# Kernel tuning notes

Hardware: AMD Instinct MI355X
Metric: run time of the kernel (lower is better)

The kernel has to match this reference:

```python
import jax, jax.numpy as jnp
import numpy as np

B, X, Y, C, H = 16, 64, 64, 256, 8
N = X * Y
EPS_LN, EPS_BN = 1e-6, 1e-5

def _conv3x3(x, w):
    return jax.lax.conv_general_dilated(x, w, (1, 1), 'SAME', dimension_numbers=('NCHW', 'OIHW', 'NCHW'))

def _bn(x, g, b, m, v):
    # eval-mode BatchNorm2d with running stats
    s = g / jnp.sqrt(v + EPS_BN)
    return x * s[None, :, None, None] + (b - m * s)[None, :, None, None]

def _ln(x, g, b):
    mu = jnp.mean(x, -1, keepdims=True)
    var = jnp.mean((x - mu) ** 2, -1, keepdims=True)
    return (x - mu) * jax.lax.rsqrt(var + EPS_LN) * g + b

def _rotate_half(x):
    x1, x2 = jnp.split(x, 2, axis=-1)
    return jnp.concatenate([-x2, x1], axis=-1)

def _rope(t, f):
    return t * jnp.cos(f) + _rotate_half(t) * jnp.sin(f)

def setup_inputs() -> dict:
    key = jax.random.key(0)
    ks = jax.random.split(key, 9)
    p = {}
    p['input'] = jax.random.normal(ks[0], (B, X, Y), jnp.float32)
    p['freq_x'] = jax.random.normal(ks[1], (B, N, C // 2), jnp.float32)
    p['freq_y'] = jax.random.normal(ks[2], (B, N, C // 2), jnp.float32)
    p['conv1_w'] = jax.random.normal(ks[3], (C, 1, 3, 3), jnp.float32) * 0.1
    p['conv2_w'] = jax.random.normal(ks[4], (C, C, 3, 3), jnp.float32) * 0.02
    for nm in ('bn1', 'bn2'):
        p[nm + '_g'] = jnp.ones((C,), jnp.float32)
        p[nm + '_b'] = jnp.zeros((C,), jnp.float32)
        p[nm + '_m'] = jnp.zeros((C,), jnp.float32)
        p[nm + '_v'] = jnp.ones((C,), jnp.float32)
    p['ln1_g'] = jnp.ones((C,), jnp.float32); p['ln1_b'] = jnp.zeros((C,), jnp.float32)
    p['ln2_g'] = jnp.ones((C,), jnp.float32); p['ln2_b'] = jnp.zeros((C,), jnp.float32)
    p['qkv_w'] = jax.random.normal(ks[5], (3 * C, C), jnp.float32) * 0.02
    p['out_w'] = jax.random.normal(ks[6], (C, C), jnp.float32) * 0.02
    p['out_b'] = jnp.zeros((C,), jnp.float32)
    p['mlp_w1'] = jax.random.normal(ks[7], (C, C), jnp.float32) * 0.02
    p['mlp_b1'] = jnp.zeros((C,), jnp.float32)
    p['mlp_w2'] = jax.random.normal(ks[8], (C, C), jnp.float32) * 0.02
    p['mlp_b2'] = jnp.zeros((C,), jnp.float32)
    return p

def reference(input, freq_x, freq_y, conv1_w, conv2_w, bn1_g, bn1_b, bn1_m, bn1_v, bn2_g, bn2_b, bn2_m, bn2_v, ln1_g, ln1_b, ln2_g, ln2_b, qkv_w, out_w, out_b, mlp_w1, mlp_b1, mlp_w2, mlp_b2):
    x4 = input[:, None]  # [B,1,X,Y]
    out = jax.nn.relu(_bn(_conv3x3(x4, conv1_w), bn1_g, bn1_b, bn1_m, bn1_v))
    out = jax.nn.relu(_bn(_conv3x3(out, conv2_w), bn2_g, bn2_b, bn2_m, bn2_v))
    feat = jax.nn.relu(x4 + out)  # broadcast residual add, [B,C,X,Y]
    inp = feat.transpose(0, 2, 3, 1).reshape(B, N, C)  # 'b h x y -> b (x y) h'
    # --- attention/MLP branch (computed as in source; its result is discarded) ---
    x = _ln(inp, ln1_g, ln1_b)
    tx, ty = x[..., :C // 2], x[..., C // 2:]
    x = jnp.concatenate([_rope(tx, freq_x), _rope(ty, freq_y)], -1)
    qkv = x @ qkv_w.T  # [B,N,3C]
    q, k, v = jnp.split(qkv, 3, -1)
    def _heads(t):
        return t.reshape(B, N, H, C // H).transpose(0, 2, 1, 3)  # [B,H,N,Dh]
    q, k, v = _heads(q), _heads(k), _heads(v)
    q = jax.nn.softmax(q, -1) * ((C // H) ** -0.5)
    k = jax.nn.softmax(k, -2)
    ctx = jnp.einsum('bhnd,bhne->bhde', k, v)   # [B,H,Dh,Dh]
    o = jnp.einsum('bhnd,bhde->bhne', q, ctx)   # [B,H,N,Dh]
    o = o.transpose(0, 2, 1, 3).reshape(B, N, C) @ out_w.T + out_b
    x = o + inp
    y = _ln(x, ln2_g, ln2_b)
    y = jax.nn.gelu(y @ mlp_w1.T + mlp_b1, approximate=False) @ mlp_w2.T + mlp_b2
    x = x + y
    # source module returns `input` (the post-stem tokens), not `x`
    return inp
```

## Files before the change

### kernel.cpp

```cpp
#include <hip/hip_runtime.h>
#include <hip/hip_bf16.h>

#define BB 16
#define XY 64
#define CC 256
#define PD 66

typedef __attribute__((ext_vector_type(8))) short short8;
typedef __attribute__((ext_vector_type(4))) float f32x4;
typedef __hip_bfloat16 bf16;

__device__ __forceinline__ void glds16(const void* g, void* l) {
  __builtin_amdgcn_global_load_lds(
      (const __attribute__((address_space(1))) void*)g,
      (__attribute__((address_space(3))) void*)l, 16, 0, 0);
}

__global__ __launch_bounds__(256) void k_conv1(
    const float* __restrict__ in,
    const float* __restrict__ w1,
    const float* __restrict__ g, const float* __restrict__ bbias,
    const float* __restrict__ m, const float* __restrict__ v,
    bf16* __restrict__ act)
{
  int blk = blockIdx.x;
  int b = blk / PD, hp = blk % PD;
  int c = threadIdx.x;
  bf16* actrow = act + (size_t)(b * PD + hp) * PD * CC;
  if (hp == 0 || hp == PD - 1) {
    for (int wp = 0; wp < PD; ++wp) actrow[wp * CC + c] = __float2bfloat16(0.f);
    return;
  }
  __shared__ float inrow[3][PD];
  int h = hp - 1;
  for (int t = threadIdx.x; t < 3 * PD; t += 256) {
    int r = t / PD, x = t % PD;
    int hr = h - 1 + r, wr = x - 1;
    inrow[r][x] = (hr >= 0 && hr < XY && wr >= 0 && wr < XY)
                      ? in[(b * XY + hr) * XY + wr] : 0.f;
  }
  __syncthreads();
  float w[9];
#pragma unroll
  for (int t = 0; t < 9; ++t) w[t] = w1[c * 9 + t];
  float s  = g[c] * rsqrtf(v[c] + 1e-5f);
  float tt = bbias[c] - m[c] * s;
  actrow[c] = __float2bfloat16(0.f);
  actrow[(PD - 1) * CC + c] = __float2bfloat16(0.f);
  for (int wp = 1; wp <= XY; ++wp) {
    float o = 0.f;
#pragma unroll
    for (int dy = 0; dy < 3; ++dy)
#pragma unroll
      for (int dx = 0; dx < 3; ++dx)
        o = fmaf(inrow[dy][wp - 1 + dx], w[dy * 3 + dx], o);
    actrow[wp * CC + c] = __float2bfloat16(fmaxf(fmaf(o, s, tt), 0.f));
  }
}

__global__ __launch_bounds__(256) void k_wb(
    const float* __restrict__ w2,
    const float* __restrict__ g, const float* __restrict__ v,
    bf16* __restrict__ Wb)
{
  int e = blockIdx.x * 256 + threadIdx.x;
  int j   = e & 7;
  int co  = (e >> 3) & 255;
  int qq  = (e >> 11) & 3;
  int c   = (e >> 13) & 7;
  int tap = e >> 16;
  int ci = c * 32 + qq * 8 + j;
  float s = g[co] * rsqrtf(v[co] + 1e-5f);
  Wb[e] = __float2bfloat16(w2[((size_t)co * CC + ci) * 9 + tap] * s);
}

__global__ __launch_bounds__(256, 3) void k_conv2(
    const bf16* __restrict__ act,
    const bf16* __restrict__ Wb,
    const float* __restrict__ in,
    const float* __restrict__ g2, const float* __restrict__ b2,
    const float* __restrict__ m2, const float* __restrict__ v2,
    float* __restrict__ out)
{
  __shared__ alignas(16) bf16 As[3 * 4 * PD * 8];
  __shared__ alignas(16) bf16 Ws[4 * CC * 8];
  __shared__ float inrow[XY];

  int blk = blockIdx.x;
  int b = blk >> 6, h = blk & 63;
  int tid = threadIdx.x;
  int lane = tid & 63, wv = tid >> 6;
  int m = lane & 15, q = lane >> 4;

  f32x4 acc[4][4];
#pragma unroll
  for (int i = 0; i < 4; ++i)
#pragma unroll
    for (int j = 0; j < 4; ++j) acc[i][j] = f32x4{0.f, 0.f, 0.f, 0.f};

  if (tid < XY) inrow[tid] = in[(b * XY + h) * XY + tid];

  const bf16* actbase = act + (size_t)(b * PD + h) * PD * CC;

  for (int c = 0; c < 8; ++c) {
    for (int tap = 0; tap < 9; ++tap) {
      const bf16* wsrc = Wb + (size_t)(tap * 8 + c) * 8192;
#pragma unroll
      for (int i = 0; i < 4; ++i) {
        int seg = wv * 4 + i;
        glds16((const char*)wsrc + seg * 1024 + lane * 16,
               (char*)Ws + seg * 1024);
      }
      if (tap == 0) {
        for (int idx = tid; idx < 792; idx += 256) {
          int qq = idx & 3, p = idx >> 2;
          int r = p / PD, wp = p % PD;
          short8 val = *(const short8*)(actbase + (size_t)(r * PD + wp) * CC + c * 32 + qq * 8);
          *(short8*)&As[((r * 4 + qq) * PD + wp) * 8] = val;
        }
      }
      __syncthreads();

      int dy = tap / 3, dx = tap % 3;
      short8 af[4], bfr[4];
#pragma unroll
      for (int mt = 0; mt < 4; ++mt)
        af[mt] = *(const short8*)&As[((dy * 4 + q) * PD + mt * 16 + m + dx) * 8];
#pragma unroll
      for (int nt = 0; nt < 4; ++nt)
        bfr[nt] = *(const short8*)&Ws[(q * CC + wv * 64 + nt * 16 + m) * 8];
#pragma unroll
      for (int mt = 0; mt < 4; ++mt)
#pragma unroll
        for (int nt = 0; nt < 4; ++nt)
          acc[mt][nt] = __builtin_amdgcn_mfma_f32_16x16x32_bf16(
              af[mt], bfr[nt], acc[mt][nt], 0, 0, 0);
      __syncthreads();
    }
  }

  float t2[4];
#pragma unroll
  for (int nt = 0; nt < 4; ++nt) {
    int co = wv * 64 + nt * 16 + m;
    float s2 = g2[co] * rsqrtf(v2[co] + 1e-5f);
    t2[nt] = b2[co] - m2[co] * s2;
  }
  float* ob = out + (size_t)(b * XY + h) * XY * CC;
#pragma unroll
  for (int mt = 0; mt < 4; ++mt)
#pragma unroll
    for (int r = 0; r < 4; ++r) {
      int wp = mt * 16 + q * 4 + r;
      float iv = inrow[wp];
#pragma unroll
      for (int nt = 0; nt < 4; ++nt) {
        int co = wv * 64 + nt * 16 + m;
        float val = fmaxf(acc[mt][nt][r] + t2[nt], 0.f);
        ob[(size_t)wp * CC + co] = fmaxf(iv + val, 0.f);
      }
    }
}

extern "C" void kernel_launch(void* const* d_in, const int* in_sizes, int n_in,
                              void* d_out, int out_size, void* d_ws, size_t ws_size,
                              hipStream_t stream) {
  const float* in_   = (const float*)d_in[0];
  const float* w1    = (const float*)d_in[3];
  const float* w2    = (const float*)d_in[4];
  const float* bn1_g = (const float*)d_in[5];
  const float* bn1_b = (const float*)d_in[6];
  const float* bn1_m = (const float*)d_in[7];
  const float* bn1_v = (const float*)d_in[8];
  const float* bn2_g = (const float*)d_in[9];
  const float* bn2_b = (const float*)d_in[10];
  const float* bn2_m = (const float*)d_in[11];
  const float* bn2_v = (const float*)d_in[12];
  float* out = (float*)d_out;

  bf16* act = (bf16*)d_ws;
  bf16* Wb  = act + (size_t)BB * PD * PD * CC;

  k_conv1<<<BB * PD, 256, 0, stream>>>(in_, w1, bn1_g, bn1_b, bn1_m, bn1_v, act);
  k_wb<<<(9 * CC * CC) / 256, 256, 0, stream>>>(w2, bn2_g, bn2_v, Wb);
  k_conv2<<<BB * XY, 256, 0, stream>>>(act, Wb, in_, bn2_g, bn2_b, bn2_m, bn2_v, out);
}
```

Measured before the change: 102.8 us.

## Restructure conv2 into 4-row tiles with triple-buffered weights and channel-group layout

The activation layout changes to channel-group-major [b][row][32 groups][66][8] so conv2 can stage A tiles directly with global_load_lds. conv1 now computes 8 channels per thread. conv2 now uses 512-thread blocks, each covering 4 output rows, with an 8x4 accumulator per wave. Weights for K=64 chunks are triple-buffered and prefetched two taps ahead, and MFMAs are interleaved with LDS loads under manual waitcnt and barriers plus setprio. Blocks are also swizzled across XCDs. The aim is to raise reuse of weights and activations and to overlap global loads with MFMA work, at the cost of higher register pressure and fragile hand-written synchronization.

```diff
diff --git a/kernel.cpp b/kernel.cpp
--- a/kernel.cpp
+++ b/kernel.cpp
@@ -4,7 +4,7 @@
 #define BB 16
 #define XY 64
 #define CC 256
-#define PD 66
+#define PR 66
 
 typedef __attribute__((ext_vector_type(8))) short short8;
 typedef __attribute__((ext_vector_type(4))) float f32x4;
@@ -24,37 +24,57 @@
     bf16* __restrict__ act)
 {
   int blk = blockIdx.x;
-  int b = blk / PD, hp = blk % PD;
-  int c = threadIdx.x;
-  bf16* actrow = act + (size_t)(b * PD + hp) * PD * CC;
-  if (hp == 0 || hp == PD - 1) {
-    for (int wp = 0; wp < PD; ++wp) actrow[wp * CC + c] = __float2bfloat16(0.f);
+  int b = blk / PR, prow = blk % PR;
+  short8* base = (short8*)(act + (size_t)(b * PR + prow) * 32 * PR * 8);
+  int tid = threadIdx.x;
+  short8 z8 = {0, 0, 0, 0, 0, 0, 0, 0};
+  if (prow == 0 || prow == PR - 1) {
+    for (int i = tid; i < 32 * PR; i += 256) base[i] = z8;
     return;
   }
-  __shared__ float inrow[3][PD];
-  int h = hp - 1;
-  for (int t = threadIdx.x; t < 3 * PD; t += 256) {
-    int r = t / PD, x = t % PD;
+  __shared__ float inrow[3][PR];
+  int h = prow - 1;
+  for (int t = tid; t < 3 * PR; t += 256) {
+    int r = t / PR, x = t % PR;
     int hr = h - 1 + r, wr = x - 1;
     inrow[r][x] = (hr >= 0 && hr < XY && wr >= 0 && wr < XY)
                       ? in[(b * XY + hr) * XY + wr] : 0.f;
   }
   __syncthreads();
-  float w[9];
-#pragma unroll
-  for (int t = 0; t < 9; ++t) w[t] = w1[c * 9 + t];
-  float s  = g[c] * rsqrtf(v[c] + 1e-5f);
-  float tt = bbias[c] - m[c] * s;
-  actrow[c] = __float2bfloat16(0.f);
-  actrow[(PD - 1) * CC + c] = __float2bfloat16(0.f);
-  for (int wp = 1; wp <= XY; ++wp) {
-    float o = 0.f;
-#pragma unroll
-    for (int dy = 0; dy < 3; ++dy)
-#pragma unroll
-      for (int dx = 0; dx < 3; ++dx)
-        o = fmaf(inrow[dy][wp - 1 + dx], w[dy * 3 + dx], o);
-    actrow[wp * CC + c] = __float2bfloat16(fmaxf(fmaf(o, s, tt), 0.f));
+  int cg = tid >> 3, w8 = tid & 7;
+  float wr_[8][9], sc[8], tc[8];
+#pragma unroll
+  for (int u = 0; u < 8; ++u) {
+    int c = cg * 8 + u;
+#pragma unroll
+    for (int t = 0; t < 9; ++t) wr_[u][t] = w1[c * 9 + t];
+    float s = g[c] * rsqrtf(v[c] + 1e-5f);
+    sc[u] = s; tc[u] = bbias[c] - m[c] * s;
+  }
+#pragma unroll
+  for (int k = 0; k < 9; ++k) {
+    int wp = w8 + 8 * k;
+    if (wp < PR) {
+      short8 outv = z8;
+      if (wp != 0 && wp != PR - 1) {
+        float o[8];
+#pragma unroll
+        for (int u = 0; u < 8; ++u) o[u] = 0.f;
+#pragma unroll
+        for (int dy = 0; dy < 3; ++dy) {
+          float i0 = inrow[dy][wp - 1], i1 = inrow[dy][wp], i2 = inrow[dy][wp + 1];
+#pragma unroll
+          for (int u = 0; u < 8; ++u)
+            o[u] += i0 * wr_[u][dy * 3] + i1 * wr_[u][dy * 3 + 1] + i2 * wr_[u][dy * 3 + 2];
+        }
+#pragma unroll
+        for (int u = 0; u < 8; ++u) {
+          bf16 hb = __float2bfloat16(fmaxf(fmaf(o[u], sc[u], tc[u]), 0.f));
+          outv[u] = *(short*)&hb;
+        }
+      }
+      base[cg * PR + wp] = outv;
+    }
   }
 }
 
@@ -66,15 +86,15 @@
   int e = blockIdx.x * 256 + threadIdx.x;
   int j   = e & 7;
   int co  = (e >> 3) & 255;
-  int qq  = (e >> 11) & 3;
-  int c   = (e >> 13) & 7;
+  int kg  = (e >> 11) & 7;
+  int c64 = (e >> 14) & 3;
   int tap = e >> 16;
-  int ci = c * 32 + qq * 8 + j;
+  int ci = c64 * 64 + kg * 8 + j;
   float s = g[co] * rsqrtf(v[co] + 1e-5f);
   Wb[e] = __float2bfloat16(w2[((size_t)co * CC + ci) * 9 + tap] * s);
 }
 
-__global__ __launch_bounds__(256, 3) void k_conv2(
+__global__ __launch_bounds__(512, 2) void k_conv2(
     const bf16* __restrict__ act,
     const bf16* __restrict__ Wb,
     const float* __restrict__ in,
@@ -82,84 +102,161 @@
     const float* __restrict__ m2, const float* __restrict__ v2,
     float* __restrict__ out)
 {
-  __shared__ alignas(16) bf16 As[3 * 4 * PD * 8];
-  __shared__ alignas(16) bf16 Ws[4 * CC * 8];
-  __shared__ float inrow[XY];
-
-  int blk = blockIdx.x;
-  int b = blk >> 6, h = blk & 63;
+  __shared__ alignas(16) bf16 Asm[3168 * 8];
+  __shared__ alignas(16) bf16 Wsm[3][2048 * 8];
+  __shared__ float inrow[4][64];
+
+  int gg = blockIdx.x;
+  int blk = (gg & 7) * 32 + (gg >> 3);
+  int b = blk >> 4, h0 = (blk & 15) << 2;
+
   int tid = threadIdx.x;
-  int lane = tid & 63, wv = tid >> 6;
+  int lane = tid & 63, wid = tid >> 6;
+  int wm = wid >> 2, wn = wid & 3;
   int m = lane & 15, q = lane >> 4;
 
-  f32x4 acc[4][4];
-#pragma unroll
-  for (int i = 0; i < 4; ++i)
+  f32x4 acc[8][4];
+#pragma unroll
+  for (int i = 0; i < 8; ++i)
 #pragma unroll
     for (int j = 0; j < 4; ++j) acc[i][j] = f32x4{0.f, 0.f, 0.f, 0.f};
 
-  if (tid < XY) inrow[tid] = in[(b * XY + h) * XY + tid];
-
-  const bf16* actbase = act + (size_t)(b * PD + h) * PD * CC;
-
-  for (int c = 0; c < 8; ++c) {
+  if (tid < 256) inrow[tid >> 6][tid & 63] = in[(b * XY + h0 + (tid >> 6)) * XY + (tid & 63)];
+  __syncthreads();
+
+  auto stageA = [&](int c64) {
+#pragma unroll
+    for (int rb = 0; rb < 7; ++rb) {
+      int sbase = rb * 512 + wid * 64;
+      if (sbase < 3168) {
+        int s = sbase + lane;
+        if (s < 3168) {
+          int r_row = s / 528;
+          int rem = s - r_row * 528;
+          int kg = rem / 66;
+          int wp = rem - kg * 66;
+          size_t gc = ((size_t)(b * PR + h0 + r_row) * 32 + (c64 * 8 + kg)) * PR + wp;
+          glds16((const char*)act + gc * 16, (char*)Asm + (size_t)sbase * 16);
+        }
+      }
+    }
+  };
+  auto stageWhalf = [&](int wblk, int buf, int half) {
+    const char* wsrc = (const char*)Wb + (size_t)wblk * 32768;
+#pragma unroll
+    for (int bt = 0; bt < 2; ++bt) {
+      int slotb = (half * 2 + bt) * 512 + wid * 64;
+      glds16(wsrc + (size_t)(slotb + lane) * 16,
+             (char*)Wsm[buf] + (size_t)slotb * 16);
+    }
+  };
+  auto loadA = [&](short8 af[2][4], int mh, int dy, int dx) {
+#pragma unroll
+    for (int kk = 0; kk < 2; ++kk)
+#pragma unroll
+      for (int t = 0; t < 4; ++t) {
+        int r = 2 * wm + mh + dy;
+        int slot = (r * 8 + kk * 4 + q) * 66 + t * 16 + m + dx;
+        af[kk][t] = *(const short8*)(Asm + (size_t)slot * 8);
+      }
+  };
+  auto loadB = [&](short8 bfr[2][2], int buf, int nh) {
+#pragma unroll
+    for (int kk = 0; kk < 2; ++kk)
+#pragma unroll
+      for (int t = 0; t < 2; ++t) {
+        int slot = (kk * 4 + q) * 256 + wn * 64 + (nh * 2 + t) * 16 + m;
+        bfr[kk][t] = *(const short8*)(Wsm[buf] + (size_t)slot * 8);
+      }
+  };
+  auto mfmaQ = [&](short8 af[2][4], short8 bfr[2][2], int mh, int nh) {
+    __builtin_amdgcn_s_setprio(1);
+#pragma unroll
+    for (int kk = 0; kk < 2; ++kk)
+#pragma unroll
+      for (int t = 0; t < 4; ++t)
+#pragma unroll
+        for (int u = 0; u < 2; ++u)
+          acc[mh * 4 + t][nh * 2 + u] = __builtin_amdgcn_mfma_f32_16x16x32_bf16(
+              af[kk][t], bfr[kk][u], acc[mh * 4 + t][nh * 2 + u], 0, 0, 0);
+    __builtin_amdgcn_s_setprio(0);
+  };
+
+  stageA(0);
+  stageWhalf(0 * 4 + 0, 0, 0); stageWhalf(0 * 4 + 0, 0, 1);
+  stageWhalf(1 * 4 + 0, 1, 0); stageWhalf(1 * 4 + 0, 1, 1);
+  asm volatile("s_waitcnt vmcnt(4)" ::: "memory");
+  __builtin_amdgcn_s_barrier();
+
+#pragma unroll 1
+  for (int c64 = 0; c64 < 4; ++c64) {
+#pragma unroll
     for (int tap = 0; tap < 9; ++tap) {
-      const bf16* wsrc = Wb + (size_t)(tap * 8 + c) * 8192;
-#pragma unroll
-      for (int i = 0; i < 4; ++i) {
-        int seg = wv * 4 + i;
-        glds16((const char*)wsrc + seg * 1024 + lane * 16,
-               (char*)Ws + seg * 1024);
-      }
-      if (tap == 0) {
-        for (int idx = tid; idx < 792; idx += 256) {
-          int qq = idx & 3, p = idx >> 2;
-          int r = p / PD, wp = p % PD;
-          short8 val = *(const short8*)(actbase + (size_t)(r * PD + wp) * CC + c * 32 + qq * 8);
-          *(short8*)&As[((r * 4 + qq) * PD + wp) * 8] = val;
-        }
-      }
-      __syncthreads();
-
-      int dy = tap / 3, dx = tap % 3;
-      short8 af[4], bfr[4];
-#pragma unroll
-      for (int mt = 0; mt < 4; ++mt)
-        af[mt] = *(const short8*)&As[((dy * 4 + q) * PD + mt * 16 + m + dx) * 8];
-#pragma unroll
-      for (int nt = 0; nt < 4; ++nt)
-        bfr[nt] = *(const short8*)&Ws[(q * CC + wv * 64 + nt * 16 + m) * 8];
-#pragma unroll
-      for (int mt = 0; mt < 4; ++mt)
-#pragma unroll
-        for (int nt = 0; nt < 4; ++nt)
-          acc[mt][nt] = __builtin_amdgcn_mfma_f32_16x16x32_bf16(
-              af[mt], bfr[nt], acc[mt][nt], 0, 0, 0);
-      __syncthreads();
+      const int dy = tap / 3, dx = tap % 3;
+      const int bi = tap % 3;
+      const int sbuf = (tap + 2) % 3;
+      const bool doW = (c64 < 3) || (tap < 7);
+      const int tap2 = (tap + 2) % 9;
+      int c64_2 = c64 + ((tap + 2) / 9);
+      int wblk2 = tap2 * 4 + c64_2;
+
+      short8 af[2][4], b0[2][2], b1[2][2];
+      loadA(af, 0, dy, dx);
+      loadB(b0, bi, 0);
+      if (doW) stageWhalf(wblk2, sbuf, 0);
+      __builtin_amdgcn_s_barrier();
+      asm volatile("s_waitcnt lgkmcnt(0)" ::: "memory");
+      __builtin_amdgcn_sched_barrier(0);
+      mfmaQ(af, b0, 0, 0);
+      __builtin_amdgcn_s_barrier();
+      loadB(b1, bi, 1);
+      if (doW) stageWhalf(wblk2, sbuf, 1);
+      __builtin_amdgcn_s_barrier();
+      asm volatile("s_waitcnt lgkmcnt(0)" ::: "memory");
+      __builtin_amdgcn_sched_barrier(0);
+      mfmaQ(af, b1, 0, 1);
+      __builtin_amdgcn_s_barrier();
+      loadA(af, 1, dy, dx);
+      __builtin_amdgcn_s_barrier();
+      asm volatile("s_waitcnt lgkmcnt(0)" ::: "memory");
+      __builtin_amdgcn_sched_barrier(0);
+      mfmaQ(af, b1, 1, 1);
+      __builtin_amdgcn_s_barrier();
+      if (tap == 8 && c64 < 3) stageA(c64 + 1);
+      __builtin_amdgcn_s_barrier();
+      __builtin_amdgcn_sched_barrier(0);
+      mfmaQ(af, b0, 1, 0);
+      if (tap == 8 || (c64 == 3 && tap >= 7))
+        asm volatile("s_waitcnt vmcnt(0)" ::: "memory");
+      else
+        asm volatile("s_waitcnt vmcnt(4)" ::: "memory");
+      __builtin_amdgcn_s_barrier();
     }
   }
 
   float t2[4];
 #pragma unroll
   for (int nt = 0; nt < 4; ++nt) {
-    int co = wv * 64 + nt * 16 + m;
+    int co = wn * 64 + nt * 16 + m;
     float s2 = g2[co] * rsqrtf(v2[co] + 1e-5f);
     t2[nt] = b2[co] - m2[co] * s2;
   }
-  float* ob = out + (size_t)(b * XY + h) * XY * CC;
-#pragma unroll
-  for (int mt = 0; mt < 4; ++mt)
+#pragma unroll
+  for (int mt = 0; mt < 8; ++mt) {
+    int orow2 = 2 * wm + (mt >> 2);
+    float* ob = out + ((size_t)(b * XY + h0 + orow2)) * XY * CC;
 #pragma unroll
     for (int r = 0; r < 4; ++r) {
-      int wp = mt * 16 + q * 4 + r;
-      float iv = inrow[wp];
+      int ocol = (mt & 3) * 16 + q * 4 + r;
+      float iv = inrow[orow2][ocol];
 #pragma unroll
       for (int nt = 0; nt < 4; ++nt) {
-        int co = wv * 64 + nt * 16 + m;
+        int co = wn * 64 + nt * 16 + m;
         float val = fmaxf(acc[mt][nt][r] + t2[nt], 0.f);
-        ob[(size_t)wp * CC + co] = fmaxf(iv + val, 0.f);
-      }
-    }
+        ob[(size_t)ocol * CC + co] = fmaxf(iv + val, 0.f);
+      }
+    }
+  }
 }
 
 extern "C" void kernel_launch(void* const* d_in, const int* in_sizes, int n_in,
@@ -179,9 +276,9 @@
   float* out = (float*)d_out;
 
   bf16* act = (bf16*)d_ws;
-  bf16* Wb  = act + (size_t)BB * PD * PD * CC;
-
-  k_conv1<<<BB * PD, 256, 0, stream>>>(in_, w1, bn1_g, bn1_b, bn1_m, bn1_v, act);
-  k_wb<<<(9 * CC * CC) / 256, 256, 0, stream>>>(w2, bn2_g, bn2_v, Wb);
-  k_conv2<<<BB * XY, 256, 0, stream>>>(act, Wb, in_, bn2_g, bn2_b, bn2_m, bn2_v, out);
-}
+  bf16* Wb  = act + (size_t)BB * PR * 32 * PR * 8;
+
+  k_conv1<<<BB * PR, 256, 0, stream>>>(in_, w1, bn1_g, bn1_b, bn1_m, bn1_v, act);
+  k_wb<<<2304, 256, 0, stream>>>(w2, bn2_g, bn2_v, Wb);
+  k_conv2<<<256, 512, 0, stream>>>(act, Wb, in_, bn2_g, bn2_b, bn2_m, bn2_v, out);
+}
```

Result: slower. 164.7 us (+60.2%).
